# Optimization experiments

Measured on AMD Instinct MI355X. Metric: run time of the kernel, lower is better.

## Reference

```python
import jax, jax.numpy as jnp
import numpy as np

EMBED_DIM = 256
NUM_HEADS = 8
HEAD_DIM = EMBED_DIM // NUM_HEADS
NUM_POINTS_LIST = [4, 4, 4, 4]
PT = sum(NUM_POINTS_LIST)  # 16 points per head, total_points = 8*16 = 128
OFFSET_SCALE = 0.5
SHAPES = np.array([[128, 128], [64, 64], [32, 32], [16, 16]], dtype=np.int32)
BS, LQ = 8, 1000


def setup_inputs() -> dict:
    key = jax.random.key(0)
    ks = jax.random.split(key, 12)
    Lv = int((SHAPES[:, 0] * SHAPES[:, 1]).sum())  # 21760
    C = EMBED_DIM
    s = 0.02
    return {
        "query": jax.random.normal(ks[0], (BS, LQ, C), jnp.float32),
        "reference_points": jax.random.uniform(ks[1], (BS, LQ, 1, 4), jnp.float32, 0.1, 0.9),
        "value": jax.random.normal(ks[2], (BS, Lv, C), jnp.float32),
        "spatial_shapes": SHAPES,  # static numpy, not traced
        "w_off": jax.random.normal(ks[3], (C, NUM_HEADS * PT * 2), jnp.float32) * s,
        "b_off": jax.random.normal(ks[4], (NUM_HEADS * PT * 2,), jnp.float32) * 0.5,
        "w_attn": jax.random.normal(ks[5], (C, NUM_HEADS * PT), jnp.float32) * s,
        "b_attn": jnp.zeros((NUM_HEADS * PT,), jnp.float32),
        "w_val": jax.random.normal(ks[6], (C, C), jnp.float32) * s,
        "b_val": jnp.zeros((C,), jnp.float32),
        "w_out": jax.random.normal(ks[7], (C, C), jnp.float32) * s,
        "b_out": jnp.zeros((C,), jnp.float32),
    }


def _sample_level(v, loc, H, W):
    """Bilinear sample (grid_sample, align_corners=False, zero padding).
    v:   [bs, nH, H*W, hd]  value features of one pyramid level
    loc: [bs, Lq, nH, P, 2] sampling locations in [0,1] (x, y)
    returns [bs, Lq, nH, P, hd]
    """
    bs, Lq, nH, P, _ = loc.shape
    hd = v.shape[-1]
    x = loc[..., 0] * W - 0.5
    y = loc[..., 1] * H - 0.5
    x0 = jnp.floor(x)
    y0 = jnp.floor(y)
    lx = x - x0
    ly = y - y0
    x0i = x0.astype(jnp.int32)
    y0i = y0.astype(jnp.int32)

    def corner(xi, yi, w):
        valid = (xi >= 0) & (xi < W) & (yi >= 0) & (yi < H)
        idx = jnp.clip(yi, 0, H - 1) * W + jnp.clip(xi, 0, W - 1)  # [bs,Lq,nH,P]
        idxf = jnp.transpose(idx, (0, 2, 1, 3)).reshape(bs, nH, Lq * P)
        g = jnp.take_along_axis(v, idxf[..., None], axis=2)  # [bs,nH,Lq*P,hd]
        wv = jnp.where(valid, w, 0.0).astype(v.dtype)
        wf = jnp.transpose(wv, (0, 2, 1, 3)).reshape(bs, nH, Lq * P, 1)
        return g * wf

    out = (corner(x0i, y0i, (1 - lx) * (1 - ly))
           + corner(x0i + 1, y0i, lx * (1 - ly))
           + corner(x0i, y0i + 1, (1 - lx) * ly)
           + corner(x0i + 1, y0i + 1, lx * ly))
    out = out.reshape(bs, nH, Lq, P, hd)
    return jnp.transpose(out, (0, 2, 1, 3, 4))


def reference(query, reference_points, value, spatial_shapes,
              w_off, b_off, w_attn, b_attn, w_val, b_val, w_out, b_out):
    shapes = np.asarray(spatial_shapes)  # static
    bs, Lq, C = query.shape
    Lv = value.shape[1]
    nH, hd, Pt = NUM_HEADS, HEAD_DIM, PT

    # value projection -> [bs, nH, Lv, hd]
    v = value @ w_val + b_val
    v = jnp.transpose(v.reshape(bs, Lv, nH, hd), (0, 2, 1, 3))

    # sampling offsets and attention weights from query
    off = (query @ w_off + b_off).reshape(bs, Lq, nH, Pt, 2)
    aw = jax.nn.softmax((query @ w_attn + b_attn).reshape(bs, Lq, nH, Pt), axis=-1)

    # reference_points: [bs, Lq, 1, 4] boxes (cx, cy, w, h) in [0,1]
    nps = jnp.asarray([1.0 / n for n in NUM_POINTS_LIST for _ in range(n)],
                      dtype=query.dtype)[:, None]  # [Pt,1]
    loc = (reference_points[:, :, None, :, :2]
           + off * nps * reference_points[:, :, None, :, 2:] * OFFSET_SCALE)  # [bs,Lq,nH,Pt,2]

    samples = []
    v_start = 0
    p_start = 0
    for l, (H, W) in enumerate(shapes):
        H, W = int(H), int(W)
        P = NUM_POINTS_LIST[l]
        v_l = jax.lax.dynamic_slice_in_dim(v, v_start, H * W, axis=2)
        loc_l = loc[:, :, :, p_start:p_start + P, :]
        samples.append(_sample_level(v_l, loc_l, H, W))
        v_start += H * W
        p_start += P
    samples = jnp.concatenate(samples, axis=3)  # [bs,Lq,nH,Pt,hd]

    out = jnp.einsum('blhp,blhpd->blhd', aw, samples).reshape(bs, Lq, C)
    return out @ w_out + b_out
```

## Files before the change

kernel.cpp:

```cpp
#include <hip/hip_runtime.h>

typedef unsigned short ushort_t;
typedef short s16x8 __attribute__((ext_vector_type(8)));
typedef float f32x4 __attribute__((ext_vector_type(4)));
typedef unsigned short u16x4 __attribute__((ext_vector_type(4)));
typedef unsigned int uint2_t __attribute__((ext_vector_type(2)));
typedef unsigned int uint4_t __attribute__((ext_vector_type(4)));

#define KDIM 256
#define BK 64
#define LDST 72
#define LV_TOTAL 21760
#define NQ 8000
#define VM_TILES2 680
#define QOA_BLOCKS 96
#define VPROJ_BLOCKS 672

__device__ inline unsigned short f2b(float f) {
  union { float f; unsigned u; } v; v.f = f;
  return (unsigned short)((v.u + 0x7fffu + ((v.u >> 16) & 1u)) >> 16);
}
__device__ inline float b2f(unsigned short h) {
  union { unsigned u; float f; } v; v.u = ((unsigned)h) << 16;
  return v.f;
}
__device__ inline unsigned pack_bf16x2(float lo, float hi) {
  union { float f; unsigned u; } a, b;
  a.f = lo; b.f = hi;
  return __builtin_amdgcn_perm(b.u + 0x8000u, a.u + 0x8000u, 0x07060302u);
}
__device__ inline unsigned short f2b_cheap(float f) {
  union { float f; unsigned u; } v; v.f = f;
  return (unsigned short)((v.u + 0x8000u) >> 16);
}

__global__ __launch_bounds__(256) void prep_weights(
    const float* __restrict__ w_off, const float* __restrict__ w_attn,
    const float* __restrict__ w_val, const float* __restrict__ w_out,
    const float* __restrict__ b_off, const float* __restrict__ b_attn,
    ushort_t* __restrict__ wt_val, ushort_t* __restrict__ wt_qoa,
    ushort_t* __restrict__ wt_out, float* __restrict__ bias_qoa,
    int* __restrict__ counters)
{
  int bid = blockIdx.x;
  int k = threadIdx.x;
  if (bid < 256) {
    int n = bid;
    wt_val[n*KDIM + k] = f2b(w_val[k*256 + n]);
  } else if (bid < 640) {
    int n = bid - 256;
    float v = (n < 256) ? w_off[k*256 + n] : w_attn[k*128 + (n - 256)];
    wt_qoa[n*KDIM + k] = f2b(v);
  } else if (bid < 896) {
    int n = bid - 640;
    wt_out[n*KDIM + k] = f2b(w_out[k*256 + n]);
  } else {
    if (k < 2) counters[k] = 0;
    for (int i = k; i < 384; i += 256)
      bias_qoa[i] = (i < 256) ? b_off[i] : b_attn[i - 256];
  }
}

__global__ __launch_bounds__(512) void merged_gemms(
    const float* __restrict__ value, const ushort_t* __restrict__ wt_val,
    const float* __restrict__ b_val, ushort_t* __restrict__ v_proj,
    const float* __restrict__ query, const ushort_t* __restrict__ wt_qoa,
    const float* __restrict__ bias_qoa, float* __restrict__ qoa,
    int* __restrict__ counters)
{
  __shared__ __align__(16) char smem[65536];
  __shared__ int s_mt2[2];
  const int tid  = threadIdx.x;
  const int wave = tid >> 6;
  const int lane = tid & 63;
  const int lrow = lane & 15;
  const int quad = lane >> 4;

  if (blockIdx.x < QOA_BLOCKS) {
    ushort_t* sA = (ushort_t*)smem;
    ushort_t* sB = (ushort_t*)(smem + 256 * LDST * 2);
    const int m0 = (blockIdx.x % 32) * 256;
    const int n0 = (blockIdx.x / 32) * 128;
    const int M = NQ, N = 384;

    f32x4 acc[2][8];
    #pragma unroll
    for (int i = 0; i < 2; ++i)
      #pragma unroll
      for (int j = 0; j < 8; ++j) acc[i][j] = {0.f, 0.f, 0.f, 0.f};

    for (int kc = 0; kc < KDIM; kc += BK) {
      #pragma unroll
      for (int i = 0; i < 8; ++i) {
        int f   = tid + i * 512;
        int row = f >> 4;
        int c4  = f & 15;
        int gr  = m0 + row;
        float4 val = {0.f, 0.f, 0.f, 0.f};
        if (gr < M) val = *(const float4*)(query + (size_t)gr * KDIM + kc + c4 * 4);
        uint2_t t;
        t.x = pack_bf16x2(val.x, val.y);
        t.y = pack_bf16x2(val.z, val.w);
        *(uint2_t*)&sA[row * LDST + c4 * 4] = t;
      }
      #pragma unroll
      for (int i = 0; i < 2; ++i) {
        int f   = tid + i * 512;
        int row = f >> 3;
        int seg = f & 7;
        s16x8 v = *(const s16x8*)(wt_qoa + (size_t)(n0 + row) * KDIM + kc + seg * 8);
        *(s16x8*)&sB[row * LDST + seg * 8] = v;
      }
      __syncthreads();
      #pragma unroll
      for (int ki = 0; ki < BK; ki += 32) {
        int krow = ki + quad * 8;
        s16x8 af[2], bfr[8];
        #pragma unroll
        for (int mt = 0; mt < 2; ++mt)
          af[mt] = *(const s16x8*)&sA[(wave * 32 + mt * 16 + lrow) * LDST + krow];
        #pragma unroll
        for (int nt = 0; nt < 8; ++nt)
          bfr[nt] = *(const s16x8*)&sB[(nt * 16 + lrow) * LDST + krow];
        #pragma unroll
        for (int mt = 0; mt < 2; ++mt)
          #pragma unroll
          for (int nt = 0; nt < 8; ++nt)
            acc[mt][nt] = __builtin_amdgcn_mfma_f32_16x16x32_bf16(
                af[mt], bfr[nt], acc[mt][nt], 0, 0, 0);
      }
      __syncthreads();
    }
    #pragma unroll
    for (int mt = 0; mt < 2; ++mt) {
      int gmb = m0 + wave * 32 + mt * 16 + quad * 4;
      #pragma unroll
      for (int nt = 0; nt < 8; ++nt) {
        int gn = n0 + nt * 16 + lrow;
        float bvv = bias_qoa[gn];
        #pragma unroll
        for (int r = 0; r < 4; ++r) {
          int gm = gmb + r;
          if (gm < M) qoa[(size_t)gm * N + gn] = acc[mt][nt][r] + bvv;
        }
      }
    }
    return;
  }

  ushort_t* sB = (ushort_t*)smem;
  const int vbid = blockIdx.x - QOA_BLOCKS;
  const int half = vbid & 1;
  const int n0   = half * 128;

  {
    const ushort_t* src = wt_val + (size_t)n0 * KDIM;
    #pragma unroll
    for (int i = 0; i < 8; ++i) {
      int g   = tid + i * 512;
      int row = g >> 5;
      int c   = g & 31;
      s16x8 v = *(const s16x8*)(src + row * KDIM + c * 8);
      *(s16x8*)&sB[row * 256 + ((c ^ (row & 7)) * 8)] = v;
    }
  }
  if (tid == 0) s_mt2[0] = atomicAdd(&counters[half], 1);
  __syncthreads();

  float bv[8];
  #pragma unroll
  for (int nt = 0; nt < 8; ++nt) bv[nt] = b_val[n0 + nt * 16 + lrow];

  const int swz = lrow & 7;

  float4 st[4][2][2];

#define LOADK(BUF, MM0, KK) do {                                              \
    const float* _p = value + (size_t)((MM0) + lrow) * KDIM + (KK) * 32 + quad * 8; \
    st[BUF][0][0] = *(const float4*)(_p);                                     \
    st[BUF][0][1] = *(const float4*)(_p + 4);                                 \
    st[BUF][1][0] = *(const float4*)(_p + 16 * KDIM);                         \
    st[BUF][1][1] = *(const float4*)(_p + 16 * KDIM + 4);                     \
  } while (0)

  int mt = s_mt2[0];
  int pb = 0;
  if (mt < VM_TILES2) {
    const int mrow = mt * 256 + wave * 32;
    LOADK(0, mrow, 0);
    LOADK(1, mrow, 1);
  }

  while (mt < VM_TILES2) {
    if (tid == 0) s_mt2[pb ^ 1] = atomicAdd(&counters[half], 1);

    const int mrow = mt * 256 + wave * 32;
    f32x4 acc[2][8];
    #pragma unroll
    for (int m = 0; m < 2; ++m)
      #pragma unroll
      for (int nt = 0; nt < 8; ++nt) acc[m][nt] = {0.f, 0.f, 0.f, 0.f};

    #pragma unroll
    for (int ks = 0; ks < 8; ++ks) {
      if (ks < 6) LOADK((ks + 2) & 3, mrow, ks + 2);
      s16x8 af[2];
      #pragma unroll
      for (int m = 0; m < 2; ++m) {
        union { uint4_t d; s16x8 v; } u;
        u.d.x = pack_bf16x2(st[ks & 3][m][0].x, st[ks & 3][m][0].y);
        u.d.y = pack_bf16x2(st[ks & 3][m][0].z, st[ks & 3][m][0].w);
        u.d.z = pack_bf16x2(st[ks & 3][m][1].x, st[ks & 3][m][1].y);
        u.d.w = pack_bf16x2(st[ks & 3][m][1].z, st[ks & 3][m][1].w);
        af[m] = u.v;
      }
      #pragma unroll
      for (int nt = 0; nt < 8; ++nt) {
        s16x8 bf = *(const s16x8*)&sB[(nt * 16 + lrow) * 256 +
                                      (((4 * ks + quad) ^ swz) * 8)];
        acc[0][nt] = __builtin_amdgcn_mfma_f32_16x16x32_bf16(af[0], bf, acc[0][nt], 0, 0, 0);
        acc[1][nt] = __builtin_amdgcn_mfma_f32_16x16x32_bf16(af[1], bf, acc[1][nt], 0, 0, 0);
      }
    }

    __syncthreads();
    const int mtn = s_mt2[pb ^ 1];

    if (mtn < VM_TILES2) {
      const int mrown = mtn * 256 + wave * 32;
      LOADK(0, mrown, 0);
      LOADK(1, mrown, 1);
    }

    #pragma unroll
    for (int m = 0; m < 2; ++m) {
      int gm = mrow + m * 16 + quad * 4;
      #pragma unroll
      for (int nt = 0; nt < 8; ++nt) {
        int gn = n0 + nt * 16 + lrow;
        #pragma unroll
        for (int r = 0; r < 4; ++r)
          v_proj[(size_t)(gm + r) * KDIM + gn] = f2b_cheap(acc[m][nt][r] + bv[nt]);
      }
    }
    mt = mtn;
    pb ^= 1;
  }
#undef LOADK
}

__global__ __launch_bounds__(256) void ms_deform_sample(
    const ushort_t* __restrict__ v,
    const float* __restrict__ qoa,
    const float* __restrict__ refp,
    float* __restrict__ outq)
{
  __shared__ float s_w[512];
  __shared__ int   s_i[512];
  const int bq  = blockIdx.x;
  const int b   = bq / 1000;
  const int tid = threadIdx.x;

  if (tid < 128) {
    const int p = tid & 15;
    const float* qrow = qoa + (size_t)bq * 384;
    float logit = qrow[256 + tid];
    float mx = logit;
    #pragma unroll
    for (int s = 8; s >= 1; s >>= 1) mx = fmaxf(mx, __shfl_xor(mx, s, 16));
    float e = __expf(logit - mx);
    float sum = e;
    #pragma unroll
    for (int s = 8; s >= 1; s >>= 1) sum += __shfl_xor(sum, s, 16);
    float aw = e / sum;

    float ox = qrow[tid * 2], oy = qrow[tid * 2 + 1];
    const float* rp = refp + (size_t)bq * 4;
    float rx = rp[0], ry = rp[1], rw = rp[2], rh = rp[3];
    const int lvl = p >> 2;
    const int HWs[4] = {128, 64, 32, 16};
    const int STs[4] = {0, 16384, 20480, 21504};
    int W = HWs[lvl], H = HWs[lvl], st = STs[lvl];
    float lx = rx + ox * 0.125f * rw;
    float ly = ry + oy * 0.125f * rh;
    float x = lx * (float)W - 0.5f;
    float y = ly * (float)H - 0.5f;
    float x0f = floorf(x), y0f = floorf(y);
    int x0 = (int)x0f, y0 = (int)y0f;
    float fx = x - x0f, fy = y - y0f;
    float wc[4] = {(1.f - fx) * (1.f - fy), fx * (1.f - fy),
                   (1.f - fx) * fy,         fx * fy};
    #pragma unroll
    for (int c = 0; c < 4; ++c) {
      int xi = x0 + (c & 1);
      int yi = y0 + (c >> 1);
      bool valid = (xi >= 0) && (xi < W) && (yi >= 0) && (yi < H);
      int xc = min(max(xi, 0), W - 1);
      int yc = min(max(yi, 0), H - 1);
      s_w[tid * 4 + c] = valid ? wc[c] * aw : 0.f;
      s_i[tid * 4 + c] = st + yc * W + xc;
    }
  }
  __syncthreads();

  const int h   = tid >> 5;
  const int l32 = tid & 31;
  const int grp = l32 >> 2;
  const int sub = l32 & 3;
  const ushort_t* vb = v + (size_t)b * LV_TOTAL * 256 + h * 32 + sub * 8;

  float wreg[8]; int ireg[8];
  #pragma unroll
  for (int i = 0; i < 8; ++i) {
    int j = h * 64 + i * 8 + grp;
    wreg[i] = s_w[j];
    ireg[i] = s_i[j];
  }
  s16x8 vv[8];
  #pragma unroll
  for (int i = 0; i < 8; ++i)
    vv[i] = *(const s16x8*)(vb + (size_t)ireg[i] * 256);

  float acc[8];
  #pragma unroll
  for (int d = 0; d < 8; ++d) acc[d] = 0.f;
  #pragma unroll
  for (int i = 0; i < 8; ++i)
    #pragma unroll
    for (int d = 0; d < 8; ++d)
      acc[d] += wreg[i] * b2f((ushort_t)vv[i][d]);

  #pragma unroll
  for (int m = 4; m <= 16; m <<= 1)
    #pragma unroll
    for (int d = 0; d < 8; ++d)
      acc[d] += __shfl_xor(acc[d], m);

  if (l32 < 4) {
    float* dst = outq + (size_t)bq * 256 + h * 32 + l32 * 8;
    float4 o0 = {acc[0], acc[1], acc[2], acc[3]};
    float4 o1 = {acc[4], acc[5], acc[6], acc[7]};
    *(float4*)dst = o0;
    *(float4*)(dst + 4) = o1;
  }
}

__global__ __launch_bounds__(256) void gemm_bf16(
    const float* __restrict__ A, const ushort_t* __restrict__ Bt,
    const float* __restrict__ bias, float* __restrict__ Cf,
    int M, int N)
{
  __shared__ ushort_t sA[128 * LDST];
  __shared__ ushort_t sB[64 * LDST];
  const int tid  = threadIdx.x;
  const int m0   = blockIdx.x * 128;
  const int n0   = blockIdx.y * 64;
  const int wave = tid >> 6;
  const int lane = tid & 63;
  const int lrow = lane & 15;
  const int quad = lane >> 4;

  f32x4 acc[2][4];
  #pragma unroll
  for (int i = 0; i < 2; ++i)
    #pragma unroll
    for (int j = 0; j < 4; ++j) acc[i][j] = {0.f, 0.f, 0.f, 0.f};

  for (int kc = 0; kc < KDIM; kc += BK) {
    #pragma unroll
    for (int i = 0; i < 8; ++i) {
      int f   = tid + i * 256;
      int row = f >> 4;
      int c4  = f & 15;
      int gr  = m0 + row;
      float4 val = {0.f, 0.f, 0.f, 0.f};
      if (gr < M) val = *(const float4*)(A + (size_t)gr * KDIM + kc + c4 * 4);
      uint2_t t;
      t.x = pack_bf16x2(val.x, val.y);
      t.y = pack_bf16x2(val.z, val.w);
      *(uint2_t*)&sA[row * LDST + c4 * 4] = t;
    }
    #pragma unroll
    for (int i = 0; i < 2; ++i) {
      int f   = tid + i * 256;
      int row = f >> 3;
      int seg = f & 7;
      s16x8 v = *(const s16x8*)(Bt + (size_t)(n0 + row) * KDIM + kc + seg * 8);
      *(s16x8*)&sB[row * LDST + seg * 8] = v;
    }
    __syncthreads();
    #pragma unroll
    for (int ki = 0; ki < BK; ki += 32) {
      int krow = ki + quad * 8;
      s16x8 af[2], bfr[4];
      #pragma unroll
      for (int mt = 0; mt < 2; ++mt)
        af[mt] = *(const s16x8*)&sA[(wave * 32 + mt * 16 + lrow) * LDST + krow];
      #pragma unroll
      for (int nt = 0; nt < 4; ++nt)
        bfr[nt] = *(const s16x8*)&sB[(nt * 16 + lrow) * LDST + krow];
      #pragma unroll
      for (int mt = 0; mt < 2; ++mt)
        #pragma unroll
        for (int nt = 0; nt < 4; ++nt)
          acc[mt][nt] = __builtin_amdgcn_mfma_f32_16x16x32_bf16(
              af[mt], bfr[nt], acc[mt][nt], 0, 0, 0);
    }
    __syncthreads();
  }
  #pragma unroll
  for (int mt = 0; mt < 2; ++mt) {
    int gmb = m0 + wave * 32 + mt * 16 + quad * 4;
    #pragma unroll
    for (int nt = 0; nt < 4; ++nt) {
      int gn = n0 + nt * 16 + lrow;
      float bvv = bias[gn];
      #pragma unroll
      for (int r = 0; r < 4; ++r) {
        int gm = gmb + r;
        if (gm < M) Cf[(size_t)gm * N + gn] = acc[mt][nt][r] + bvv;
      }
    }
  }
}

extern "C" void kernel_launch(void* const* d_in, const int* in_sizes, int n_in,
                              void* d_out, int out_size, void* d_ws, size_t ws_size,
                              hipStream_t stream) {
  const float* query  = (const float*)d_in[0];
  const float* refp   = (const float*)d_in[1];
  const float* value  = (const float*)d_in[2];
  const float* w_off  = (const float*)d_in[4];
  const float* b_off  = (const float*)d_in[5];
  const float* w_attn = (const float*)d_in[6];
  const float* b_attn = (const float*)d_in[7];
  const float* w_val  = (const float*)d_in[8];
  const float* b_val  = (const float*)d_in[9];
  const float* w_out  = (const float*)d_in[10];
  const float* b_out  = (const float*)d_in[11];
  float* out = (float*)d_out;

  char* ws = (char*)d_ws;
  const size_t WS_NEEDED = 110069760;
  if (ws_size < WS_NEEDED) return;
  ushort_t* wt_val   = (ushort_t*)(ws);
  ushort_t* wt_qoa   = (ushort_t*)(ws + 131072);
  ushort_t* wt_out   = (ushort_t*)(ws + 327680);
  float*    bias_qoa = (float*)   (ws + 458752);
  int*      counters = (int*)     (ws + 460288);
  ushort_t* v_proj   = (ushort_t*)(ws + 460800);
  float*    qoa      = (float*)   (ws + 89589760);
  float*    outq     = (float*)   (ws + 101877760);

  prep_weights<<<897, 256, 0, stream>>>(w_off, w_attn, w_val, w_out, b_off, b_attn,
                                        wt_val, wt_qoa, wt_out, bias_qoa, counters);
  merged_gemms<<<QOA_BLOCKS + VPROJ_BLOCKS, 512, 0, stream>>>(
      value, wt_val, b_val, v_proj, query, wt_qoa, bias_qoa, qoa, counters);
  ms_deform_sample<<<NQ, 256, 0, stream>>>(v_proj, qoa, refp, outq);
  gemm_bf16<<<dim3(63, 4), 256, 0, stream>>>(outq, wt_out, b_out, out, NQ, 256);
}
```

Measured before the change: 375.3 us.

## Transpose MFMA operands for vectorized epilogue stores and pipeline tile prefetch across barrier

```diff
diff --git a/kernel.cpp b/kernel.cpp
--- a/kernel.cpp
+++ b/kernel.cpp
@@ -3,7 +3,6 @@
 typedef unsigned short ushort_t;
 typedef short s16x8 __attribute__((ext_vector_type(8)));
 typedef float f32x4 __attribute__((ext_vector_type(4)));
-typedef unsigned short u16x4 __attribute__((ext_vector_type(4)));
 typedef unsigned int uint2_t __attribute__((ext_vector_type(2)));
 typedef unsigned int uint4_t __attribute__((ext_vector_type(4)));
 
@@ -14,7 +13,7 @@
 #define NQ 8000
 #define VM_TILES2 680
 #define QOA_BLOCKS 96
-#define VPROJ_BLOCKS 672
+#define VPROJ_BLOCKS 512
 
 __device__ inline unsigned short f2b(float f) {
   union { float f; unsigned u; } v; v.f = f;
@@ -28,10 +27,6 @@
   union { float f; unsigned u; } a, b;
   a.f = lo; b.f = hi;
   return __builtin_amdgcn_perm(b.u + 0x8000u, a.u + 0x8000u, 0x07060302u);
-}
-__device__ inline unsigned short f2b_cheap(float f) {
-  union { float f; unsigned u; } v; v.f = f;
-  return (unsigned short)((v.u + 0x8000u) >> 16);
 }
 
 __global__ __launch_bounds__(256) void prep_weights(
@@ -69,7 +64,7 @@
     int* __restrict__ counters)
 {
   __shared__ __align__(16) char smem[65536];
-  __shared__ int s_mt2[2];
+  __shared__ int s_mtR[3];
   const int tid  = threadIdx.x;
   const int wave = tid >> 6;
   const int lane = tid & 63;
@@ -127,21 +122,21 @@
           #pragma unroll
           for (int nt = 0; nt < 8; ++nt)
             acc[mt][nt] = __builtin_amdgcn_mfma_f32_16x16x32_bf16(
-                af[mt], bfr[nt], acc[mt][nt], 0, 0, 0);
+                bfr[nt], af[mt], acc[mt][nt], 0, 0, 0);
       }
       __syncthreads();
     }
     #pragma unroll
     for (int mt = 0; mt < 2; ++mt) {
-      int gmb = m0 + wave * 32 + mt * 16 + quad * 4;
-      #pragma unroll
-      for (int nt = 0; nt < 8; ++nt) {
-        int gn = n0 + nt * 16 + lrow;
-        float bvv = bias_qoa[gn];
+      const int gm = m0 + wave * 32 + mt * 16 + lrow;
+      if (gm < M) {
         #pragma unroll
-        for (int r = 0; r < 4; ++r) {
-          int gm = gmb + r;
-          if (gm < M) qoa[(size_t)gm * N + gn] = acc[mt][nt][r] + bvv;
+        for (int nt = 0; nt < 8; ++nt) {
+          const int gn = n0 + nt * 16 + quad * 4;
+          const float4 b4 = *(const float4*)(bias_qoa + gn);
+          float4 o = {acc[mt][nt][0] + b4.x, acc[mt][nt][1] + b4.y,
+                      acc[mt][nt][2] + b4.z, acc[mt][nt][3] + b4.w};
+          *(float4*)(qoa + (size_t)gm * N + gn) = o;
         }
       }
     }
@@ -164,12 +159,8 @@
       *(s16x8*)&sB[row * 256 + ((c ^ (row & 7)) * 8)] = v;
     }
   }
-  if (tid == 0) s_mt2[0] = atomicAdd(&counters[half], 1);
+  if (tid == 0) s_mtR[0] = atomicAdd(&counters[half], 1);
   __syncthreads();
-
-  float bv[8];
-  #pragma unroll
-  for (int nt = 0; nt < 8; ++nt) bv[nt] = b_val[n0 + nt * 16 + lrow];
 
   const int swz = lrow & 7;
 
@@ -183,27 +174,40 @@
     st[BUF][1][1] = *(const float4*)(_p + 16 * KDIM + 4);                     \
   } while (0)
 
-  int mt = s_mt2[0];
-  int pb = 0;
+  int mt = s_mtR[0];
+  int sl = 0;
   if (mt < VM_TILES2) {
+    const int mr = mt * 256 + wave * 32;
+    LOADK(0, mr, 0);
+    LOADK(1, mr, 1);
+  }
+
+  while (mt < VM_TILES2) {
+    const int sln = (sl == 2) ? 0 : sl + 1;
+    int t = 0;
+    if (tid == 0) t = atomicAdd(&counters[half], 1);
     const int mrow = mt * 256 + wave * 32;
-    LOADK(0, mrow, 0);
-    LOADK(1, mrow, 1);
-  }
-
-  while (mt < VM_TILES2) {
-    if (tid == 0) s_mt2[pb ^ 1] = atomicAdd(&counters[half], 1);
-
-    const int mrow = mt * 256 + wave * 32;
+
     f32x4 acc[2][8];
     #pragma unroll
     for (int m = 0; m < 2; ++m)
       #pragma unroll
       for (int nt = 0; nt < 8; ++nt) acc[m][nt] = {0.f, 0.f, 0.f, 0.f};
 
+    int mtn = VM_TILES2;
     #pragma unroll
     for (int ks = 0; ks < 8; ++ks) {
-      if (ks < 6) LOADK((ks + 2) & 3, mrow, ks + 2);
+      if (ks == 2) { if (tid == 0) s_mtR[sln] = t; }
+      if (ks == 4) {
+        asm volatile("s_waitcnt lgkmcnt(0)" ::: "memory");
+        __builtin_amdgcn_s_barrier();
+      }
+      if (ks == 6) mtn = s_mtR[sln];
+      if (ks < 6) {
+        LOADK((ks + 2) & 3, mrow, ks + 2);
+      } else if (mtn < VM_TILES2) {
+        LOADK(ks - 6, mtn * 256 + wave * 32, ks - 6);
+      }
       s16x8 af[2];
       #pragma unroll
       for (int m = 0; m < 2; ++m) {
@@ -218,33 +222,26 @@
       for (int nt = 0; nt < 8; ++nt) {
         s16x8 bf = *(const s16x8*)&sB[(nt * 16 + lrow) * 256 +
                                       (((4 * ks + quad) ^ swz) * 8)];
-        acc[0][nt] = __builtin_amdgcn_mfma_f32_16x16x32_bf16(af[0], bf, acc[0][nt], 0, 0, 0);
-        acc[1][nt] = __builtin_amdgcn_mfma_f32_16x16x32_bf16(af[1], bf, acc[1][nt], 0, 0, 0);
-      }
-    }
-
-    __syncthreads();
-    const int mtn = s_mt2[pb ^ 1];
-
-    if (mtn < VM_TILES2) {
-      const int mrown = mtn * 256 + wave * 32;
-      LOADK(0, mrown, 0);
-      LOADK(1, mrown, 1);
+        acc[0][nt] = __builtin_amdgcn_mfma_f32_16x16x32_bf16(bf, af[0], acc[0][nt], 0, 0, 0);
+        acc[1][nt] = __builtin_amdgcn_mfma_f32_16x16x32_bf16(bf, af[1], acc[1][nt], 0, 0, 0);
+      }
     }
 
     #pragma unroll
     for (int m = 0; m < 2; ++m) {
-      int gm = mrow + m * 16 + quad * 4;
+      const int gm = mrow + m * 16 + lrow;
       #pragma unroll
       for (int nt = 0; nt < 8; ++nt) {
-        int gn = n0 + nt * 16 + lrow;
-        #pragma unroll
-        for (int r = 0; r < 4; ++r)
-          v_proj[(size_t)(gm + r) * KDIM + gn] = f2b_cheap(acc[m][nt][r] + bv[nt]);
+        const int gn = n0 + nt * 16 + quad * 4;
+        const float4 b4 = *(const float4*)(b_val + gn);
+        uint2_t u;
+        u.x = pack_bf16x2(acc[m][nt][0] + b4.x, acc[m][nt][1] + b4.y);
+        u.y = pack_bf16x2(acc[m][nt][2] + b4.z, acc[m][nt][3] + b4.w);
+        *(uint2_t*)(v_proj + (size_t)gm * 256 + gn) = u;
       }
     }
     mt = mtn;
-    pb ^= 1;
+    sl = sln;
   }
 #undef LOADK
 }
@@ -404,21 +401,21 @@
         #pragma unroll
         for (int nt = 0; nt < 4; ++nt)
           acc[mt][nt] = __builtin_amdgcn_mfma_f32_16x16x32_bf16(
-              af[mt], bfr[nt], acc[mt][nt], 0, 0, 0);
+              bfr[nt], af[mt], acc[mt][nt], 0, 0, 0);
     }
     __syncthreads();
   }
   #pragma unroll
   for (int mt = 0; mt < 2; ++mt) {
-    int gmb = m0 + wave * 32 + mt * 16 + quad * 4;
-    #pragma unroll
-    for (int nt = 0; nt < 4; ++nt) {
-      int gn = n0 + nt * 16 + lrow;
-      float bvv = bias[gn];
-      #pragma unroll
-      for (int r = 0; r < 4; ++r) {
-        int gm = gmb + r;
-        if (gm < M) Cf[(size_t)gm * N + gn] = acc[mt][nt][r] + bvv;
+    const int gm = m0 + wave * 32 + mt * 16 + lrow;
+    if (gm < M) {
+      #pragma unroll
+      for (int nt = 0; nt < 4; ++nt) {
+        const int gn = n0 + nt * 16 + quad * 4;
+        const float4 b4 = *(const float4*)(bias + gn);
+        float4 o = {acc[mt][nt][0] + b4.x, acc[mt][nt][1] + b4.y,
+                    acc[mt][nt][2] + b4.z, acc[mt][nt][3] + b4.w};
+        *(float4*)(Cf + (size_t)gm * N + gn) = o;
       }
     }
   }
```

Measured after the change: 370.8 us. Within noise of the previous version (-1.2%).
